# Kernel tuning notes

Measured on AMD Instinct MI355X. Metric: run time of the kernel, lower is better.

The kernel has to match this reference:

```python
import jax, jax.numpy as jnp
import numpy as np

H = 2048      # hidden_size
NH = 16       # num heads
HD = H // NH  # head_dim = 128


def setup_inputs() -> dict:
    key = jax.random.key(0)
    ks = jax.random.split(key, 5)
    x = jax.random.normal(ks[0], (2, 2048, H), dtype=jnp.float32)
    # qkv_proj: Linear(H, 3H) with bias; out_proj: Linear(H, H) with bias
    s = 1.0 / np.sqrt(H)
    w_qkv = jax.random.uniform(ks[1], (3 * H, H), jnp.float32, -s, s)
    b_qkv = jax.random.uniform(ks[2], (3 * H,), jnp.float32, -s, s)
    w_out = jax.random.uniform(ks[3], (H, H), jnp.float32, -s, s)
    b_out = jax.random.uniform(ks[4], (H,), jnp.float32, -s, s)
    return {"x": x, "w_qkv": w_qkv, "b_qkv": b_qkv, "w_out": w_out, "b_out": b_out}


def reference(x, w_qkv, b_qkv, w_out, b_out):
    b, s, _ = x.shape
    # fused QKV projection: [b, s, 3H]
    xqkv = jnp.einsum('bsh,oh->bso', x, w_qkv) + b_qkv
    xqkv = xqkv.reshape(b, s, 3, NH, HD)
    q = xqkv[:, :, 0].transpose(0, 2, 1, 3)  # [b, nh, s, hd]
    k = xqkv[:, :, 1].transpose(0, 2, 1, 3)
    v = xqkv[:, :, 2].transpose(0, 2, 1, 3)
    # non-causal SDPA (attn_mask=None, is_causal=False)
    scores = jnp.einsum('bhqd,bhkd->bhqk', q, k) / np.sqrt(HD).astype(np.float32)
    attn = jax.nn.softmax(scores, axis=-1)
    out = jnp.einsum('bhqk,bhkd->bhqd', attn, v)
    out = out.transpose(0, 2, 1, 3).reshape(b, s, NH * HD)
    return jnp.einsum('bsh,oh->bso', out, w_out) + b_out
```

## Files before the change

kernel.cpp:

```cpp
#include <hip/hip_runtime.h>
#include <hip/hip_bf16.h>


typedef __bf16 bf16x8 __attribute__((ext_vector_type(8)));
typedef float f32x4 __attribute__((ext_vector_type(4)));
typedef unsigned short ushort8_t __attribute__((ext_vector_type(8)));
typedef unsigned short ushort4_t __attribute__((ext_vector_type(4)));

__device__ __forceinline__ unsigned short f2bf(float f) {
  unsigned int u = __float_as_uint(f);
  u += 0x7fffu + ((u >> 16) & 1u);
  return (unsigned short)(u >> 16);
}

__device__ __forceinline__ unsigned int pk2bf(float lo, float hi) {
  unsigned int a = (__float_as_uint(lo) + 0x8000u) >> 16;
  unsigned int b = (__float_as_uint(hi) + 0x8000u) & 0xffff0000u;
  return a | b;
}

__device__ __forceinline__ float fexp2(float x) {
#if __has_builtin(__builtin_amdgcn_exp2f)
  return __builtin_amdgcn_exp2f(x);
#else
  return exp2f(x);
#endif
}

__device__ __forceinline__ f32x4 mfma16(bf16x8 a, bf16x8 b, f32x4 c) {
  return __builtin_amdgcn_mfma_f32_16x16x32_bf16(a, b, c, 0, 0, 0);
}

__device__ __forceinline__ void gload_lds16(const void* g, void* lds) {
  __builtin_amdgcn_global_load_lds(
      (const __attribute__((address_space(1))) unsigned int*)g,
      (__attribute__((address_space(3))) unsigned int*)lds, 16, 0, 0);
}

__global__ __launch_bounds__(256) void f32_to_bf16_k(const float* __restrict__ in,
                                                     unsigned short* __restrict__ out,
                                                     int n) {
  int i = (blockIdx.x * 256 + threadIdx.x) * 8;
  if (i >= n) return;
  float4 a = *(const float4*)(in + i);
  float4 b = *(const float4*)(in + i + 4);
  ushort8_t o;
  o[0] = f2bf(a.x); o[1] = f2bf(a.y); o[2] = f2bf(a.z); o[3] = f2bf(a.w);
  o[4] = f2bf(b.x); o[5] = f2bf(b.y); o[6] = f2bf(b.z); o[7] = f2bf(b.w);
  *(ushort8_t*)(out + i) = o;
}

template <int OUT_MODE>
__global__ __launch_bounds__(256) void gemm_nt(const unsigned short* __restrict__ A,
                                               const unsigned short* __restrict__ B,
                                               const float* __restrict__ bias,
                                               void* __restrict__ Cout,
                                               int Ns, int K) {
  __shared__ __attribute__((aligned(16))) unsigned short As[128 * 64];
  __shared__ __attribute__((aligned(16))) unsigned short Bs[128 * 64];
  const int tid = threadIdx.x;
  const int lane = tid & 63;
  const int wv = tid >> 6;
  const int wm = wv >> 1, wn = wv & 1;
  const int lr = lane & 15, lg = lane >> 4;
  const int m0 = blockIdx.y * 128, n0 = blockIdx.x * 128;

  f32x4 acc[4][4];
#pragma unroll
  for (int i = 0; i < 4; ++i)
#pragma unroll
    for (int j = 0; j < 4; ++j) acc[i][j] = (f32x4){0.f, 0.f, 0.f, 0.f};

  for (int kt = 0; kt < K; kt += 64) {
    __syncthreads();
#pragma unroll
    for (int i = 0; i < 4; ++i) {
      int c = i * 256 + tid;
      int r = c >> 3;
      int lc = (c & 7) ^ (r & 7);
      gload_lds16(A + (size_t)(m0 + r) * K + kt + lc * 8, &As[c * 8]);
      gload_lds16(B + (size_t)(n0 + r) * K + kt + lc * 8, &Bs[c * 8]);
    }
    __syncthreads();
#pragma unroll
    for (int kk = 0; kk < 64; kk += 32) {
      bf16x8 af[4], bf[4];
#pragma unroll
      for (int i = 0; i < 4; ++i) {
        int pcA = ((kk >> 3) + lg) ^ (lr & 7);
        af[i] = *(const bf16x8*)&As[(wm * 64 + i * 16 + lr) * 64 + pcA * 8];
        bf[i] = *(const bf16x8*)&Bs[(wn * 64 + i * 16 + lr) * 64 + pcA * 8];
      }
#pragma unroll
      for (int i = 0; i < 4; ++i)
#pragma unroll
        for (int j = 0; j < 4; ++j) acc[i][j] = mfma16(af[i], bf[j], acc[i][j]);
    }
  }

#pragma unroll
  for (int j = 0; j < 4; ++j) {
    int n = n0 + wn * 64 + j * 16 + lr;
    float bv = bias[n];
#pragma unroll
    for (int i = 0; i < 4; ++i) {
      int mbase = m0 + wm * 64 + i * 16 + lg * 4;
      if (OUT_MODE == 2) {
        int hh = n >> 7, dd = n & 127;
        int b = mbase >> 11, s = mbase & 2047;
        ushort4_t o4;
#pragma unroll
        for (int r = 0; r < 4; ++r) o4[r] = f2bf(acc[i][j][r] + bv);
        *(ushort4_t*)&((unsigned short*)Cout)[((size_t)((b * 16 + hh) * 128 + dd)) * 2048 + s] = o4;
      } else {
#pragma unroll
        for (int r = 0; r < 4; ++r) {
          float v = acc[i][j][r] + bv;
          if (OUT_MODE == 1)
            ((unsigned short*)Cout)[(size_t)(mbase + r) * Ns + n] = f2bf(v);
          else
            ((float*)Cout)[(size_t)(mbase + r) * Ns + n] = v;
        }
      }
    }
  }
}

__global__ __launch_bounds__(256, 2) void flash_attn(const unsigned short* __restrict__ qkv,
                                                     const unsigned short* __restrict__ vT,
                                                     unsigned short* __restrict__ attnb) {
  __shared__ __attribute__((aligned(16))) unsigned short Ks[64 * 128];
  __shared__ __attribute__((aligned(16))) unsigned short Vt[128 * 64];

  const int tid = threadIdx.x;
  const int lane = tid & 63;
  const int w = tid >> 6;
  const int bh = blockIdx.y;
  const int b = bh >> 4, h = bh & 15;
  const int q0 = blockIdx.x * 128;
  const int lr = lane & 15, lg = lane >> 4;
  const float cs = 0.08838834764831845f * 1.44269504088896340f;

  bf16x8 qf[2][4];
#pragma unroll
  for (int g = 0; g < 2; ++g) {
    int m = b * 2048 + q0 + w * 32 + g * 16 + lr;
    const unsigned short* qrow = qkv + (size_t)m * 6144 + h * 128;
#pragma unroll
    for (int kb = 0; kb < 4; ++kb) qf[g][kb] = *(const bf16x8*)(qrow + kb * 32 + lg * 8);
  }

  float l_i[2] = {0.f, 0.f};
  f32x4 O[2][8];
#pragma unroll
  for (int g = 0; g < 2; ++g)
#pragma unroll
    for (int nb = 0; nb < 8; ++nb) O[g][nb] = (f32x4){0.f, 0.f, 0.f, 0.f};

  const unsigned short* vbase = vT + (size_t)bh * 128 * 2048;
  const int srcA = lr + ((lg & 1) ? 32 : 0);
  const int srcB = srcA + 16;
  const bool hi = (lg >> 1) != 0;

  for (int t = 0; t < 32; ++t) {
    const int s0k = t * 64;
    __syncthreads();
    const int krow = b * 2048 + s0k;
#pragma unroll
    for (int i = 0; i < 4; ++i) {
      int c = i * 256 + tid;
      int r = c >> 4;
      int lc = (c & 15) ^ (r & 15);
      gload_lds16(qkv + (size_t)(krow + r) * 6144 + 2048 + h * 128 + lc * 8, &Ks[c * 8]);
    }
#pragma unroll
    for (int i = 0; i < 4; ++i) {
      int c = i * 256 + tid;
      int r = c >> 3;
      int lc = (c & 7) ^ (r & 7);
      gload_lds16(vbase + (size_t)r * 2048 + s0k + lc * 8, &Vt[c * 8]);
    }
    __syncthreads();

    f32x4 sc[2][4];
#pragma unroll
    for (int g = 0; g < 2; ++g)
#pragma unroll
      for (int cb = 0; cb < 4; ++cb) sc[g][cb] = (f32x4){0.f, 0.f, 0.f, 0.f};
#pragma unroll
    for (int cb = 0; cb < 4; ++cb) {
#pragma unroll
      for (int kb = 0; kb < 4; ++kb) {
        int pc = (kb * 4 + lg) ^ lr;
        bf16x8 kf = *(const bf16x8*)&Ks[(cb * 16 + lr) * 128 + pc * 8];
        sc[0][cb] = mfma16(kf, qf[0][kb], sc[0][cb]);
        sc[1][cb] = mfma16(kf, qf[1][kb], sc[1][cb]);
      }
    }

    unsigned int pk[2][4][2];
#pragma unroll
    for (int g = 0; g < 2; ++g) {
      float rs = 0.f;
#pragma unroll
      for (int cb = 0; cb < 4; ++cb) {
        float p0 = fexp2(sc[g][cb][0] * cs);
        float p1 = fexp2(sc[g][cb][1] * cs);
        float p2 = fexp2(sc[g][cb][2] * cs);
        float p3 = fexp2(sc[g][cb][3] * cs);
        rs += (p0 + p1) + (p2 + p3);
        pk[g][cb][0] = pk2bf(p0, p1);
        pk[g][cb][1] = pk2bf(p2, p3);
      }
      rs += __shfl_xor(rs, 16, 64);
      rs += __shfl_xor(rs, 32, 64);
      l_i[g] += rs;
    }

#pragma unroll
    for (int kb2 = 0; kb2 < 2; ++kb2) {
      bf16x8 pf[2];
#pragma unroll
      for (int g = 0; g < 2; ++g) {
        unsigned int x0a = __shfl((int)pk[g][2 * kb2 + 0][0], srcA, 64);
        unsigned int x0b = __shfl((int)pk[g][2 * kb2 + 1][0], srcA, 64);
        unsigned int x1a = __shfl((int)pk[g][2 * kb2 + 0][1], srcA, 64);
        unsigned int x1b = __shfl((int)pk[g][2 * kb2 + 1][1], srcA, 64);
        unsigned int x2a = __shfl((int)pk[g][2 * kb2 + 0][0], srcB, 64);
        unsigned int x2b = __shfl((int)pk[g][2 * kb2 + 1][0], srcB, 64);
        unsigned int x3a = __shfl((int)pk[g][2 * kb2 + 0][1], srcB, 64);
        unsigned int x3b = __shfl((int)pk[g][2 * kb2 + 1][1], srcB, 64);
        uint4 u;
        u.x = hi ? x0b : x0a;
        u.y = hi ? x1b : x1a;
        u.z = hi ? x2b : x2a;
        u.w = hi ? x3b : x3a;
        pf[g] = *(bf16x8*)&u;
      }
#pragma unroll
      for (int nb = 0; nb < 8; ++nb) {
        int pc = (kb2 * 4 + lg) ^ (lr & 7);
        bf16x8 vtf = *(const bf16x8*)&Vt[(nb * 16 + lr) * 64 + pc * 8];
        O[0][nb] = mfma16(vtf, pf[0], O[0][nb]);
        O[1][nb] = mfma16(vtf, pf[1], O[1][nb]);
      }
    }
  }

#pragma unroll
  for (int g = 0; g < 2; ++g) {
    int m = b * 2048 + q0 + w * 32 + g * 16 + lr;
    float inv = 1.0f / l_i[g];
    unsigned short* orow = attnb + (size_t)m * 2048 + h * 128;
#pragma unroll
    for (int nb = 0; nb < 8; ++nb) {
      ushort4_t o4;
#pragma unroll
      for (int r = 0; r < 4; ++r) o4[r] = f2bf(O[g][nb][r] * inv);
      *(ushort4_t*)&orow[nb * 16 + lg * 4] = o4;
    }
  }
}

extern "C" void kernel_launch(void* const* d_in, const int* in_sizes, int n_in,
                              void* d_out, int out_size, void* d_ws, size_t ws_size,
                              hipStream_t stream) {
  const float* x = (const float*)d_in[0];
  const float* w_qkv = (const float*)d_in[1];
  const float* b_qkv = (const float*)d_in[2];
  const float* w_out = (const float*)d_in[3];
  const float* b_out = (const float*)d_in[4];
  float* out = (float*)d_out;

  char* ws = (char*)d_ws;
  unsigned short* xb = (unsigned short*)ws;
  unsigned short* attnb = xb;
  unsigned short* wqkvb = (unsigned short*)(ws + (16u << 20));
  unsigned short* woutb = wqkvb;
  unsigned short* qkvb = (unsigned short*)(ws + (40u << 20));
  unsigned short* vT = (unsigned short*)(ws + (88u << 20));

  f32_to_bf16_k<<<8388608 / 2048, 256, 0, stream>>>(x, xb, 8388608);
  f32_to_bf16_k<<<12582912 / 2048, 256, 0, stream>>>(w_qkv, wqkvb, 12582912);

  gemm_nt<1><<<dim3(32, 32), 256, 0, stream>>>(xb, wqkvb, b_qkv, qkvb, 6144, 2048);
  gemm_nt<2><<<dim3(16, 32), 256, 0, stream>>>(xb, wqkvb + (size_t)4096 * 2048,
                                               b_qkv + 4096, vT, 2048, 2048);

  f32_to_bf16_k<<<4194304 / 2048, 256, 0, stream>>>(w_out, woutb, 4194304);

  flash_attn<<<dim3(16, 32), 256, 0, stream>>>(qkvb, vT, attnb);

  gemm_nt<0><<<dim3(16, 32), 256, 0, stream>>>(attnb, woutb, b_out, out, 2048, 2048);
}
```

Baseline: 404.1 us.

## Split flash attention KV range across warp pairs and reduce partial outputs in LDS

Each block now covers 64 queries instead of 128. Its two warp pairs each process half of the key sequence into separate K buffers in shared memory, and the grid doubles to launch more blocks. V tiles are read straight from global memory instead of being staged in LDS, and launch bounds go up to 4 blocks per CU. The partial O and row sums are combined through LDS at the end. This is meant to raise parallelism and occupancy, at the cost of uncoalesced global V reads and an extra reduction step, with no max subtraction so the split stays valid.

```diff
diff --git a/kernel.cpp b/kernel.cpp
--- a/kernel.cpp
+++ b/kernel.cpp
@@ -126,73 +126,70 @@
   }
 }
 
-__global__ __launch_bounds__(256, 2) void flash_attn(const unsigned short* __restrict__ qkv,
+__global__ __launch_bounds__(256, 4) void flash_attn(const unsigned short* __restrict__ qkv,
                                                      const unsigned short* __restrict__ vT,
                                                      unsigned short* __restrict__ attnb) {
-  __shared__ __attribute__((aligned(16))) unsigned short Ks[64 * 128];
-  __shared__ __attribute__((aligned(16))) unsigned short Vt[128 * 64];
+  __shared__ __attribute__((aligned(16))) unsigned short Ks[2][64 * 128];
+  __shared__ float lbuf[2][2][16];
 
   const int tid = threadIdx.x;
   const int lane = tid & 63;
   const int w = tid >> 6;
+  const int qw = w & 1;
+  const int g = w >> 1;
+  const int ltid = tid & 127;
   const int bh = blockIdx.y;
   const int b = bh >> 4, h = bh & 15;
-  const int q0 = blockIdx.x * 128;
+  const int q0 = blockIdx.x * 64;
   const int lr = lane & 15, lg = lane >> 4;
   const float cs = 0.08838834764831845f * 1.44269504088896340f;
 
   bf16x8 qf[2][4];
 #pragma unroll
-  for (int g = 0; g < 2; ++g) {
-    int m = b * 2048 + q0 + w * 32 + g * 16 + lr;
+  for (int j = 0; j < 2; ++j) {
+    int m = b * 2048 + q0 + qw * 32 + j * 16 + lr;
     const unsigned short* qrow = qkv + (size_t)m * 6144 + h * 128;
 #pragma unroll
-    for (int kb = 0; kb < 4; ++kb) qf[g][kb] = *(const bf16x8*)(qrow + kb * 32 + lg * 8);
+    for (int kb = 0; kb < 4; ++kb) qf[j][kb] = *(const bf16x8*)(qrow + kb * 32 + lg * 8);
   }
 
   float l_i[2] = {0.f, 0.f};
   f32x4 O[2][8];
 #pragma unroll
-  for (int g = 0; g < 2; ++g)
-#pragma unroll
-    for (int nb = 0; nb < 8; ++nb) O[g][nb] = (f32x4){0.f, 0.f, 0.f, 0.f};
+  for (int j = 0; j < 2; ++j)
+#pragma unroll
+    for (int nb = 0; nb < 8; ++nb) O[j][nb] = (f32x4){0.f, 0.f, 0.f, 0.f};
 
   const unsigned short* vbase = vT + (size_t)bh * 128 * 2048;
+  unsigned short* myKs = Ks[g];
   const int srcA = lr + ((lg & 1) ? 32 : 0);
   const int srcB = srcA + 16;
   const bool hi = (lg >> 1) != 0;
 
-  for (int t = 0; t < 32; ++t) {
-    const int s0k = t * 64;
+  for (int it = 0; it < 16; ++it) {
+    const int s0k = (g * 16 + it) * 64;
     __syncthreads();
     const int krow = b * 2048 + s0k;
 #pragma unroll
-    for (int i = 0; i < 4; ++i) {
-      int c = i * 256 + tid;
+    for (int i = 0; i < 8; ++i) {
+      int c = i * 128 + ltid;
       int r = c >> 4;
       int lc = (c & 15) ^ (r & 15);
-      gload_lds16(qkv + (size_t)(krow + r) * 6144 + 2048 + h * 128 + lc * 8, &Ks[c * 8]);
-    }
-#pragma unroll
-    for (int i = 0; i < 4; ++i) {
-      int c = i * 256 + tid;
-      int r = c >> 3;
-      int lc = (c & 7) ^ (r & 7);
-      gload_lds16(vbase + (size_t)r * 2048 + s0k + lc * 8, &Vt[c * 8]);
+      gload_lds16(qkv + (size_t)(krow + r) * 6144 + 2048 + h * 128 + lc * 8, &myKs[c * 8]);
     }
     __syncthreads();
 
     f32x4 sc[2][4];
 #pragma unroll
-    for (int g = 0; g < 2; ++g)
-#pragma unroll
-      for (int cb = 0; cb < 4; ++cb) sc[g][cb] = (f32x4){0.f, 0.f, 0.f, 0.f};
+    for (int j = 0; j < 2; ++j)
+#pragma unroll
+      for (int cb = 0; cb < 4; ++cb) sc[j][cb] = (f32x4){0.f, 0.f, 0.f, 0.f};
 #pragma unroll
     for (int cb = 0; cb < 4; ++cb) {
 #pragma unroll
       for (int kb = 0; kb < 4; ++kb) {
         int pc = (kb * 4 + lg) ^ lr;
-        bf16x8 kf = *(const bf16x8*)&Ks[(cb * 16 + lr) * 128 + pc * 8];
+        bf16x8 kf = *(const bf16x8*)&myKs[(cb * 16 + lr) * 128 + pc * 8];
         sc[0][cb] = mfma16(kf, qf[0][kb], sc[0][cb]);
         sc[1][cb] = mfma16(kf, qf[1][kb], sc[1][cb]);
       }
@@ -200,64 +197,94 @@
 
     unsigned int pk[2][4][2];
 #pragma unroll
-    for (int g = 0; g < 2; ++g) {
+    for (int j = 0; j < 2; ++j) {
       float rs = 0.f;
 #pragma unroll
       for (int cb = 0; cb < 4; ++cb) {
-        float p0 = fexp2(sc[g][cb][0] * cs);
-        float p1 = fexp2(sc[g][cb][1] * cs);
-        float p2 = fexp2(sc[g][cb][2] * cs);
-        float p3 = fexp2(sc[g][cb][3] * cs);
+        float p0 = fexp2(sc[j][cb][0] * cs);
+        float p1 = fexp2(sc[j][cb][1] * cs);
+        float p2 = fexp2(sc[j][cb][2] * cs);
+        float p3 = fexp2(sc[j][cb][3] * cs);
         rs += (p0 + p1) + (p2 + p3);
-        pk[g][cb][0] = pk2bf(p0, p1);
-        pk[g][cb][1] = pk2bf(p2, p3);
+        pk[j][cb][0] = pk2bf(p0, p1);
+        pk[j][cb][1] = pk2bf(p2, p3);
       }
       rs += __shfl_xor(rs, 16, 64);
       rs += __shfl_xor(rs, 32, 64);
-      l_i[g] += rs;
+      l_i[j] += rs;
     }
 
 #pragma unroll
     for (int kb2 = 0; kb2 < 2; ++kb2) {
       bf16x8 pf[2];
 #pragma unroll
-      for (int g = 0; g < 2; ++g) {
-        unsigned int x0a = __shfl((int)pk[g][2 * kb2 + 0][0], srcA, 64);
-        unsigned int x0b = __shfl((int)pk[g][2 * kb2 + 1][0], srcA, 64);
-        unsigned int x1a = __shfl((int)pk[g][2 * kb2 + 0][1], srcA, 64);
-        unsigned int x1b = __shfl((int)pk[g][2 * kb2 + 1][1], srcA, 64);
-        unsigned int x2a = __shfl((int)pk[g][2 * kb2 + 0][0], srcB, 64);
-        unsigned int x2b = __shfl((int)pk[g][2 * kb2 + 1][0], srcB, 64);
-        unsigned int x3a = __shfl((int)pk[g][2 * kb2 + 0][1], srcB, 64);
-        unsigned int x3b = __shfl((int)pk[g][2 * kb2 + 1][1], srcB, 64);
+      for (int j = 0; j < 2; ++j) {
+        unsigned int x0a = __shfl((int)pk[j][2 * kb2 + 0][0], srcA, 64);
+        unsigned int x0b = __shfl((int)pk[j][2 * kb2 + 1][0], srcA, 64);
+        unsigned int x1a = __shfl((int)pk[j][2 * kb2 + 0][1], srcA, 64);
+        unsigned int x1b = __shfl((int)pk[j][2 * kb2 + 1][1], srcA, 64);
+        unsigned int x2a = __shfl((int)pk[j][2 * kb2 + 0][0], srcB, 64);
+        unsigned int x2b = __shfl((int)pk[j][2 * kb2 + 1][0], srcB, 64);
+        unsigned int x3a = __shfl((int)pk[j][2 * kb2 + 0][1], srcB, 64);
+        unsigned int x3b = __shfl((int)pk[j][2 * kb2 + 1][1], srcB, 64);
         uint4 u;
         u.x = hi ? x0b : x0a;
         u.y = hi ? x1b : x1a;
         u.z = hi ? x2b : x2a;
         u.w = hi ? x3b : x3a;
-        pf[g] = *(bf16x8*)&u;
+        pf[j] = *(bf16x8*)&u;
       }
 #pragma unroll
       for (int nb = 0; nb < 8; ++nb) {
-        int pc = (kb2 * 4 + lg) ^ (lr & 7);
-        bf16x8 vtf = *(const bf16x8*)&Vt[(nb * 16 + lr) * 64 + pc * 8];
+        bf16x8 vtf = *(const bf16x8*)(vbase + (size_t)(nb * 16 + lr) * 2048 +
+                                      s0k + kb2 * 32 + lg * 8);
         O[0][nb] = mfma16(vtf, pf[0], O[0][nb]);
         O[1][nb] = mfma16(vtf, pf[1], O[1][nb]);
       }
     }
   }
 
-#pragma unroll
-  for (int g = 0; g < 2; ++g) {
-    int m = b * 2048 + q0 + w * 32 + g * 16 + lr;
-    float inv = 1.0f / l_i[g];
-    unsigned short* orow = attnb + (size_t)m * 2048 + h * 128;
-#pragma unroll
-    for (int nb = 0; nb < 8; ++nb) {
-      ushort4_t o4;
-#pragma unroll
-      for (int r = 0; r < 4; ++r) o4[r] = f2bf(O[g][nb][r] * inv);
-      *(ushort4_t*)&orow[nb * 16 + lg * 4] = o4;
+  float* scr = (float*)&Ks[0][0];
+#pragma unroll 1
+  for (int r2 = 0; r2 < 2; ++r2) {
+    __syncthreads();
+    if (g == 1) {
+#pragma unroll
+      for (int j = 0; j < 2; ++j)
+#pragma unroll
+        for (int nbi = 0; nbi < 4; ++nbi)
+          *(f32x4*)&scr[(((qw * 2 + j) * 4 + nbi) * 64 + lane) * 4] = O[j][r2 * 4 + nbi];
+      if (r2 == 0 && lg == 0) {
+        lbuf[qw][0][lr] = l_i[0];
+        lbuf[qw][1][lr] = l_i[1];
+      }
+    }
+    __syncthreads();
+    if (g == 0) {
+#pragma unroll
+      for (int j = 0; j < 2; ++j)
+#pragma unroll
+        for (int nbi = 0; nbi < 4; ++nbi) {
+          f32x4 p = *(const f32x4*)&scr[(((qw * 2 + j) * 4 + nbi) * 64 + lane) * 4];
+#pragma unroll
+          for (int r = 0; r < 4; ++r) O[j][r2 * 4 + nbi][r] += p[r];
+        }
+    }
+  }
+
+  if (g == 0) {
+#pragma unroll
+    for (int j = 0; j < 2; ++j) {
+      int m = b * 2048 + q0 + qw * 32 + j * 16 + lr;
+      float inv = 1.0f / (l_i[j] + lbuf[qw][j][lr]);
+      unsigned short* orow = attnb + (size_t)m * 2048 + h * 128;
+#pragma unroll
+      for (int nb = 0; nb < 8; ++nb) {
+        ushort4_t o4;
+#pragma unroll
+        for (int r = 0; r < 4; ++r) o4[r] = f2bf(O[j][nb][r] * inv);
+        *(ushort4_t*)&orow[nb * 16 + lg * 4] = o4;
+      }
     }
   }
 }
@@ -289,7 +316,7 @@
 
   f32_to_bf16_k<<<4194304 / 2048, 256, 0, stream>>>(w_out, woutb, 4194304);
 
-  flash_attn<<<dim3(16, 32), 256, 0, stream>>>(qkvb, vT, attnb);
+  flash_attn<<<dim3(32, 32), 256, 0, stream>>>(qkvb, vT, attnb);
 
   gemm_nt<0><<<dim3(16, 32), 256, 0, stream>>>(attnb, woutb, b_out, out, 2048, 2048);
 }
```

After: 1.091 ms. 170% more time.
